# Optimization experiments

Hardware: AMD Instinct MI355X
Metric: run time of the kernel (lower is better)

## Reference

```python
import jax, jax.numpy as jnp
import numpy as np

LEVELS = 256
DIST = 5  # distances=[5]
# angle 0 => pixel pair (r, c) and (r, c + DIST)


def setup_inputs() -> dict:
    key = jax.random.key(0)
    img = jax.random.uniform(key, (64, 3, 512, 512), dtype=jnp.float32)
    return {"img": img}


def _glcm_features(gray_idx):
    """gray_idx: [B, H, W] int32 in [0, 255]. Returns [B, 5] float32 features."""
    B = gray_idx.shape[0]
    i = gray_idx[:, :, :-DIST]  # reference pixel
    j = gray_idx[:, :, DIST:]   # neighbor at angle 0, distance 5
    flat = (i * LEVELS + j).reshape(B, -1)

    def hist_one(f):
        return jnp.zeros(LEVELS * LEVELS, jnp.float32).at[f].add(1.0)

    glcm = jax.vmap(hist_one)(flat).reshape(B, LEVELS, LEVELS)
    glcm = glcm + jnp.swapaxes(glcm, 1, 2)          # symmetric=True
    glcm = glcm / jnp.sum(glcm, axis=(1, 2), keepdims=True)  # normed=True

    lvl = jnp.arange(LEVELS, dtype=jnp.float32)
    di = lvl[:, None] - lvl[None, :]                # (i - j), [L, L]

    contrast = jnp.sum(glcm * (di * di), axis=(1, 2))
    dissimilarity = jnp.sum(glcm * jnp.abs(di), axis=(1, 2))
    homogeneity = jnp.sum(glcm / (1.0 + di * di), axis=(1, 2))
    energy = jnp.sqrt(jnp.sum(glcm * glcm, axis=(1, 2)))  # sqrt(ASM)

    # correlation (skimage graycoprops formula)
    mu_i = jnp.sum(glcm * lvl[None, :, None], axis=(1, 2))  # [B]
    mu_j = jnp.sum(glcm * lvl[None, None, :], axis=(1, 2))
    ci = lvl[None, :, None] - mu_i[:, None, None]
    cj = lvl[None, None, :] - mu_j[:, None, None]
    var_i = jnp.sum(glcm * ci * ci, axis=(1, 2))
    var_j = jnp.sum(glcm * cj * cj, axis=(1, 2))
    cov = jnp.sum(glcm * ci * cj, axis=(1, 2))
    std = jnp.sqrt(var_i * var_j)
    corr = jnp.where(std < 1e-15, 1.0, cov / jnp.maximum(std, 1e-15))

    return jnp.stack([contrast, dissimilarity, homogeneity, energy, corr], axis=1)


def reference(img):
    # to_pil_image: float [0,1] -> uint8 via mul(255) + truncation
    q = jnp.clip(jnp.floor(img * 255.0), 0.0, 255.0)  # [B, 3, H, W]
    # cv2 RGB2GRAY: 0.299 R + 0.587 G + 0.114 B, rounded to uint8
    gray = 0.299 * q[:, 0] + 0.587 * q[:, 1] + 0.114 * q[:, 2]
    gray_idx = jnp.clip(jnp.round(gray), 0.0, 255.0).astype(jnp.int32)  # [B, H, W]

    feats = _glcm_features(gray_idx)  # [B, 5]

    # per-image min-max normalize over the 5 features, quantize to uint8, RGB, to_tensor
    fmin = jnp.min(feats, axis=1, keepdims=True)
    fmax = jnp.max(feats, axis=1, keepdims=True)
    fn = (feats - fmin) / (fmax - fmin)
    q8 = jnp.floor(fn * 255.0)                       # uint8 truncation
    out = jnp.broadcast_to(q8[:, None, :], (feats.shape[0], 3, 5)) / 255.0
    return out
```

## Files before the change

### kernel.cpp

```cpp
#include <hip/hip_runtime.h>
#include <stdint.h>

#define NLEV   256
#define DIST   5
#define NB     64
#define NH     512
#define NW     512
#define PLANE  (NH*NW)
#define NPAIRS (NH*(NW-DIST))
#define NPARTS 4


__global__ __launch_bounds__(1024) void k_grayhist(const float* __restrict__ img,
                                                   uint32_t* __restrict__ hist8,
                                                   double* __restrict__ lin) {
    __shared__ uint32_t lh[32768];
    __shared__ double sred[6][16];
    const int part = blockIdx.x & 3;
    const int b    = blockIdx.x >> 2;
    const int t    = threadIdx.x;
    const int w    = t >> 6;
    const int lane = t & 63;

    {
        uint4* lh4 = (uint4*)lh;
        for (int k = t; k < 8192; k += 1024) lh4[k] = make_uint4(0, 0, 0, 0);
    }
    __syncthreads();

    const int row0 = part * 128;
#pragma unroll 1
    for (int it = 0; it < 8; ++it) {
        const int row = row0 + (it << 4) + w;
        const size_t ibase = ((size_t)(b * 3) * NH + row) * NW;
        const float4* pR = (const float4*)(img + ibase);
        const float4* pG = (const float4*)(img + ibase + PLANE);
        const float4* pB = (const float4*)(img + ibase + 2 * (size_t)PLANE);
        float4 r0 = pR[2 * lane], r1 = pR[2 * lane + 1];
        float4 g0 = pG[2 * lane], g1 = pG[2 * lane + 1];
        float4 b0 = pB[2 * lane], b1 = pB[2 * lane + 1];

        float rr[8] = {r0.x, r0.y, r0.z, r0.w, r1.x, r1.y, r1.z, r1.w};
        float gg[8] = {g0.x, g0.y, g0.z, g0.w, g1.x, g1.y, g1.z, g1.w};
        float bb[8] = {b0.x, b0.y, b0.z, b0.w, b1.x, b1.y, b1.z, b1.w};

        uint32_t gi[8];
#pragma unroll
        for (int k = 0; k < 8; ++k) {
            float qr = fminf(fmaxf(floorf(__fmul_rn(rr[k], 255.0f)), 0.0f), 255.0f);
            float qg = fminf(fmaxf(floorf(__fmul_rn(gg[k], 255.0f)), 0.0f), 255.0f);
            float qb = fminf(fmaxf(floorf(__fmul_rn(bb[k], 255.0f)), 0.0f), 255.0f);
            float gy = __fadd_rn(__fadd_rn(__fmul_rn(0.299f, qr),
                                           __fmul_rn(0.587f, qg)),
                                 __fmul_rn(0.114f, qb));
            int v = (int)rintf(gy);
            gi[k] = (uint32_t)(v < 0 ? 0 : (v > 255 ? 255 : v));
        }
        uint32_t w0 = gi[0] | (gi[1] << 8) | (gi[2] << 16) | (gi[3] << 24);
        uint32_t w1 = gi[4] | (gi[5] << 8) | (gi[6] << 16) | (gi[7] << 24);
        uint32_t nw0 = __shfl(w0, lane + 1, 64);
        uint32_t nw1 = __shfl(w1, lane + 1, 64);
        uint32_t jlo = (w1 >> 8) | (nw0 << 24);
        uint32_t jhi = (nw0 >> 8) | (nw1 << 24);
        const int np = (lane == 63) ? 3 : 8;
#pragma unroll
        for (int k = 0; k < 8; ++k) {
            if (k < np) {
                uint32_t j = ((k < 4) ? (jlo >> (8 * k)) : (jhi >> (8 * (k - 4)))) & 255u;
                uint32_t bin1 = (gi[k] << 8) | j;
                uint32_t bin2 = (j << 8) | gi[k];
                atomicAdd(&lh[bin1 >> 1], 1u << ((bin1 & 1u) << 4));
                atomicAdd(&lh[bin2 >> 1], 1u << ((bin2 & 1u) << 4));
            }
        }
    }
    __syncthreads();

    uint32_t* dst = hist8 + (((size_t)(part * NB + b)) << 14);
    unsigned long long M_con = 0, M_dis = 0, M_si = 0, M_sii = 0, M_sij = 0;
    float M_hom = 0.0f;
#pragma unroll 1
    for (int it = 0; it < 16; ++it) {
        int widx = (it << 10) + t;
        uint2 v2 = *(const uint2*)(lh + 2 * widx);
        uint32_t s[4] = {v2.x & 0xFFFFu, v2.x >> 16, v2.y & 0xFFFFu, v2.y >> 16};
        dst[widx] = s[0] | (s[1] << 8) | (s[2] << 16) | (s[3] << 24);
        int bin0 = widx << 2;
        int i  = bin0 >> 8;
        int j0 = bin0 & 255;
#pragma unroll
        for (int e = 0; e < 4; ++e) {
            uint32_t c = s[e];
            int j = j0 + e;
            int d = i - j;
            uint32_t ad = (uint32_t)(d < 0 ? -d : d);
            M_con += (unsigned long long)c * (ad * ad);
            M_dis += (unsigned long long)c * ad;
            M_si  += (unsigned long long)c * (uint32_t)i;
            M_sii += (unsigned long long)c * (uint32_t)(i * i);
            M_sij += (unsigned long long)c * (uint32_t)(i * j);
            M_hom += (float)c * __builtin_amdgcn_rcpf((float)(1u + ad * ad));
        }
    }

    double acc[6] = {(double)M_con, (double)M_dis, (double)M_hom,
                     (double)M_si, (double)M_sii, (double)M_sij};
#pragma unroll
    for (int a = 0; a < 6; ++a) {
#pragma unroll
        for (int off = 32; off; off >>= 1)
            acc[a] += __shfl_down(acc[a], off, 64);
    }
    if (lane == 0) {
#pragma unroll
        for (int a = 0; a < 6; ++a) sred[a][w] = acc[a];
    }
    __syncthreads();
    if (t < 6) {
        double s = 0.0;
#pragma unroll
        for (int k = 0; k < 16; ++k) s += sred[t][k];
        lin[(size_t)(part * NB + b) * 6 + t] = s;
    }
}

__global__ __launch_bounds__(256) void k_energy(const uint32_t* __restrict__ hist8,
                                                double* __restrict__ en) {
    const int b = blockIdx.x >> 2;
    const int q = blockIdx.x & 3;
    const int t = threadIdx.x;

    unsigned long long E = 0;
#pragma unroll
    for (int it = 0; it < 4; ++it) {
        const int idx = (q << 10) + (it << 8) + t;
        uint4 tot = make_uint4(0, 0, 0, 0);
#pragma unroll
        for (int p = 0; p < NPARTS; ++p) {
            const uint4* hp = (const uint4*)(hist8 + (((size_t)(p * NB + b)) << 14));
            uint4 v = hp[idx];
            tot.x += v.x; tot.y += v.y;
            tot.z += v.z; tot.w += v.w;
        }
        uint32_t wds[4] = {tot.x, tot.y, tot.z, tot.w};
#pragma unroll
        for (int k = 0; k < 4; ++k) {
#pragma unroll
            for (int e = 0; e < 4; ++e) {
                uint32_t s = (wds[k] >> (e << 3)) & 255u;
                E += (unsigned long long)s * s;
            }
        }
    }

    double x = (double)E;
#pragma unroll
    for (int off = 32; off; off >>= 1)
        x += __shfl_down(x, off, 64);
    __shared__ double sr[4];
    if ((t & 63) == 0) sr[t >> 6] = x;
    __syncthreads();
    if (t == 0) en[blockIdx.x] = sr[0] + sr[1] + sr[2] + sr[3];
}

__global__ __launch_bounds__(64) void k_final(const double* __restrict__ lin,
                                              const double* __restrict__ en,
                                              float* __restrict__ out) {
    int b = blockIdx.x;
    if (threadIdx.x == 0) {
        double v[6] = {0, 0, 0, 0, 0, 0};
#pragma unroll
        for (int p = 0; p < NPARTS; ++p)
#pragma unroll
            for (int a = 0; a < 6; ++a)
                v[a] += lin[(size_t)(p * NB + b) * 6 + a];
        double E = en[b * 4] + en[b * 4 + 1] + en[b * 4 + 2] + en[b * 4 + 3];

        const double T = 2.0 * (double)NPAIRS;
        double contrast = v[0] / T;
        double dissim   = v[1] / T;
        double homog    = v[2] / T;
        double energy   = sqrt(E) / T;
        double mu    = v[3] / T;
        double var   = v[4] / T - mu * mu;
        double cov   = v[5] / T - mu * mu;
        double sd    = sqrt(var * var);
        double corr  = (sd < 1e-15) ? 1.0 : cov / fmax(sd, 1e-15);

        float f[5] = {(float)contrast, (float)dissim, (float)homog,
                      (float)energy, (float)corr};
        float mn = f[0], mx = f[0];
#pragma unroll
        for (int k = 1; k < 5; ++k) { mn = fminf(mn, f[k]); mx = fmaxf(mx, f[k]); }
        float rng = mx - mn;
#pragma unroll
        for (int k = 0; k < 5; ++k) {
            float fn = (f[k] - mn) / rng;
            float q8 = floorf(__fmul_rn(fn, 255.0f));
            float val = q8 / 255.0f;
            out[b * 15 + 0 * 5 + k] = val;
            out[b * 15 + 1 * 5 + k] = val;
            out[b * 15 + 2 * 5 + k] = val;
        }
    }
}

extern "C" void kernel_launch(void* const* d_in, const int* in_sizes, int n_in,
                              void* d_out, int out_size, void* d_ws, size_t ws_size,
                              hipStream_t stream) {
    const float* img = (const float*)d_in[0];
    float* out = (float*)d_out;

    uint32_t* hist8 = (uint32_t*)d_ws;
    double* lin = (double*)((char*)d_ws + ((size_t)16 << 20));
    double* en  = lin + (size_t)NPARTS * NB * 6;

    k_grayhist<<<NB * NPARTS, 1024, 0, stream>>>(img, hist8, lin);
    k_energy<<<NB * 4, 256, 0, stream>>>(hist8, en);
    k_final<<<NB, 64, 0, stream>>>(lin, en, out);
}
```

Measured before the change: 56.33 us.

## Use symmetric upper-triangle histogram, per-pair moments, and register prefetch of rows

The histogram kernel now does one shared atomic per pixel pair into a single (min,max) upper-triangle bin instead of two symmetric atomics. It accumulates the linear moments (contrast, dissimilarity, homogeneity, sums for correlation) directly per pair in registers, which removes the post-histogram scan over all 65536 bins. It also prefetches the next row's RGB data into registers while the current row is processed. Only tiles touching the upper triangle are written out, and the energy kernel skips the lower triangle, rebuilding the symmetric sum of squares as 2*(E+diag). The final kernel rescales the moments for the halved counting. The cost is extra per-pair ALU work and more register pressure.

After: 49.87 us. 1.13x faster.

```diff
diff --git a/kernel.cpp b/kernel.cpp
--- a/kernel.cpp
+++ b/kernel.cpp
@@ -29,20 +29,31 @@
     __syncthreads();
 
     const int row0 = part * 128;
+    const size_t ibase = ((size_t)(b * 3) * NH + row0 + w) * NW;
+    const float4* pR = (const float4*)(img + ibase);
+    const float4* pG = pR + (PLANE / 4);
+    const float4* pB = pR + (PLANE / 2);
+
+    uint32_t Mcon = 0, Mdis = 0, Msi = 0, Msii = 0, Msij = 0;
+    float Mhom = 0.0f;
+
+    float4 cr0 = pR[2 * lane], cr1 = pR[2 * lane + 1];
+    float4 cg0 = pG[2 * lane], cg1 = pG[2 * lane + 1];
+    float4 cb0 = pB[2 * lane], cb1 = pB[2 * lane + 1];
+
 #pragma unroll 1
     for (int it = 0; it < 8; ++it) {
-        const int row = row0 + (it << 4) + w;
-        const size_t ibase = ((size_t)(b * 3) * NH + row) * NW;
-        const float4* pR = (const float4*)(img + ibase);
-        const float4* pG = (const float4*)(img + ibase + PLANE);
-        const float4* pB = (const float4*)(img + ibase + 2 * (size_t)PLANE);
-        float4 r0 = pR[2 * lane], r1 = pR[2 * lane + 1];
-        float4 g0 = pG[2 * lane], g1 = pG[2 * lane + 1];
-        float4 b0 = pB[2 * lane], b1 = pB[2 * lane + 1];
-
-        float rr[8] = {r0.x, r0.y, r0.z, r0.w, r1.x, r1.y, r1.z, r1.w};
-        float gg[8] = {g0.x, g0.y, g0.z, g0.w, g1.x, g1.y, g1.z, g1.w};
-        float bb[8] = {b0.x, b0.y, b0.z, b0.w, b1.x, b1.y, b1.z, b1.w};
+        float4 nr0, nr1, ng0, ng1, nb0, nb1;
+        if (it < 7) {
+            const int o = 2048 * (it + 1) + 2 * lane;
+            nr0 = pR[o]; nr1 = pR[o + 1];
+            ng0 = pG[o]; ng1 = pG[o + 1];
+            nb0 = pB[o]; nb1 = pB[o + 1];
+        }
+
+        float rr[8] = {cr0.x, cr0.y, cr0.z, cr0.w, cr1.x, cr1.y, cr1.z, cr1.w};
+        float gg[8] = {cg0.x, cg0.y, cg0.z, cg0.w, cg1.x, cg1.y, cg1.z, cg1.w};
+        float bb[8] = {cb0.x, cb0.y, cb0.z, cb0.w, cb1.x, cb1.y, cb1.z, cb1.w};
 
         uint32_t gi[8];
 #pragma unroll
@@ -67,44 +78,27 @@
         for (int k = 0; k < 8; ++k) {
             if (k < np) {
                 uint32_t j = ((k < 4) ? (jlo >> (8 * k)) : (jhi >> (8 * (k - 4)))) & 255u;
-                uint32_t bin1 = (gi[k] << 8) | j;
-                uint32_t bin2 = (j << 8) | gi[k];
-                atomicAdd(&lh[bin1 >> 1], 1u << ((bin1 & 1u) << 4));
-                atomicAdd(&lh[bin2 >> 1], 1u << ((bin2 & 1u) << 4));
+                uint32_t ii = gi[k];
+                uint32_t m = ii < j ? ii : j;
+                uint32_t M = ii < j ? j : ii;
+                uint32_t bin = (m << 8) | M;
+                atomicAdd(&lh[bin >> 1], 1u << ((bin & 1u) << 4));
+                int d = (int)ii - (int)j;
+                uint32_t ad = (uint32_t)(d < 0 ? -d : d);
+                Mcon += ad * ad;
+                Mdis += ad;
+                Msi  += ii + j;
+                Msii += ii * ii + j * j;
+                Msij += ii * j;
+                Mhom += __builtin_amdgcn_rcpf((float)(1u + ad * ad));
             }
         }
-    }
-    __syncthreads();
-
-    uint32_t* dst = hist8 + (((size_t)(part * NB + b)) << 14);
-    unsigned long long M_con = 0, M_dis = 0, M_si = 0, M_sii = 0, M_sij = 0;
-    float M_hom = 0.0f;
-#pragma unroll 1
-    for (int it = 0; it < 16; ++it) {
-        int widx = (it << 10) + t;
-        uint2 v2 = *(const uint2*)(lh + 2 * widx);
-        uint32_t s[4] = {v2.x & 0xFFFFu, v2.x >> 16, v2.y & 0xFFFFu, v2.y >> 16};
-        dst[widx] = s[0] | (s[1] << 8) | (s[2] << 16) | (s[3] << 24);
-        int bin0 = widx << 2;
-        int i  = bin0 >> 8;
-        int j0 = bin0 & 255;
-#pragma unroll
-        for (int e = 0; e < 4; ++e) {
-            uint32_t c = s[e];
-            int j = j0 + e;
-            int d = i - j;
-            uint32_t ad = (uint32_t)(d < 0 ? -d : d);
-            M_con += (unsigned long long)c * (ad * ad);
-            M_dis += (unsigned long long)c * ad;
-            M_si  += (unsigned long long)c * (uint32_t)i;
-            M_sii += (unsigned long long)c * (uint32_t)(i * i);
-            M_sij += (unsigned long long)c * (uint32_t)(i * j);
-            M_hom += (float)c * __builtin_amdgcn_rcpf((float)(1u + ad * ad));
-        }
-    }
-
-    double acc[6] = {(double)M_con, (double)M_dis, (double)M_hom,
-                     (double)M_si, (double)M_sii, (double)M_sij};
+
+        cr0 = nr0; cr1 = nr1; cg0 = ng0; cg1 = ng1; cb0 = nb0; cb1 = nb1;
+    }
+
+    double acc[6] = {(double)Mcon, (double)Mdis, (double)Mhom,
+                     (double)Msi, (double)Msii, (double)Msij};
 #pragma unroll
     for (int a = 0; a < 6; ++a) {
 #pragma unroll
@@ -121,6 +115,18 @@
 #pragma unroll
         for (int k = 0; k < 16; ++k) s += sred[t][k];
         lin[(size_t)(part * NB + b) * 6 + t] = s;
+    }
+
+    uint32_t* dst = hist8 + (((size_t)(part * NB + b)) << 14);
+#pragma unroll 1
+    for (int it = 0; it < 16; ++it) {
+        int wd = (it << 10) + t;
+        uint2 v2 = *(const uint2*)(lh + 2 * wd);
+        uint32_t pk = (v2.x & 0xFFu) | ((v2.x >> 8) & 0xFF00u)
+                    | ((v2.y & 0xFFu) << 16) | ((v2.y >> 16) << 24);
+        int iw  = wd >> 6;
+        int j0w = (wd & 63) << 2;
+        if ((j0w | 31) >= iw) dst[wd] = pk;
     }
 }
 
@@ -130,10 +136,13 @@
     const int q = blockIdx.x & 3;
     const int t = threadIdx.x;
 
-    unsigned long long E = 0;
+    unsigned long long E = 0, Ediag = 0;
 #pragma unroll
     for (int it = 0; it < 4; ++it) {
         const int idx = (q << 10) + (it << 8) + t;
+        const int i  = idx >> 4;
+        const int j0 = (idx & 15) << 4;
+        if (j0 + 15 < i) continue;
         uint4 tot = make_uint4(0, 0, 0, 0);
 #pragma unroll
         for (int p = 0; p < NPARTS; ++p) {
@@ -148,12 +157,14 @@
 #pragma unroll
             for (int e = 0; e < 4; ++e) {
                 uint32_t s = (wds[k] >> (e << 3)) & 255u;
-                E += (unsigned long long)s * s;
+                unsigned long long s2 = (unsigned long long)s * s;
+                E += s2;
+                if (j0 + (k << 2) + e == i) Ediag += s2;
             }
         }
     }
 
-    double x = (double)E;
+    double x = (double)(2ull * (E + Ediag));
 #pragma unroll
     for (int off = 32; off; off >>= 1)
         x += __shfl_down(x, off, 64);
@@ -177,13 +188,13 @@
         double E = en[b * 4] + en[b * 4 + 1] + en[b * 4 + 2] + en[b * 4 + 3];
 
         const double T = 2.0 * (double)NPAIRS;
-        double contrast = v[0] / T;
-        double dissim   = v[1] / T;
-        double homog    = v[2] / T;
+        double contrast = 2.0 * v[0] / T;
+        double dissim   = 2.0 * v[1] / T;
+        double homog    = 2.0 * v[2] / T;
         double energy   = sqrt(E) / T;
         double mu    = v[3] / T;
         double var   = v[4] / T - mu * mu;
-        double cov   = v[5] / T - mu * mu;
+        double cov   = 2.0 * v[5] / T - mu * mu;
         double sd    = sqrt(var * var);
         double corr  = (sd < 1e-15) ? 1.0 : cov / fmax(sd, 1e-15);
 
```
